# Kernel tuning notes

Hardware: AMD Instinct MI355X
Metric: run time of the kernel (lower is better)

The kernel has to match this reference:

```python
import jax, jax.numpy as jnp
import numpy as np

B, S, V, NC3, ND = 128, 200, 64, 4000, 100


def setup_inputs() -> dict:
    key = jax.random.key(0)
    ks = jax.random.split(key, 20)
    s = 0.05
    n = lambda k, shp: jax.random.normal(k, shp, dtype=jnp.float32) * s
    return {
        "c3_seq": jax.random.randint(ks[0], (B, S), 0, NC3),
        "d_seq": jax.random.randint(ks[1], (B, S), 0, ND),
        "r_seq": jax.random.randint(ks[2], (B, S), 0, 2),
        "v_c3": n(ks[3], (V,)),
        "D_w": n(ks[4], (ND, 1)),
        "v_d": n(ks[5], (V,)),
        "R_w": n(ks[6], (2, V)),
        "W_ih": n(ks[7], (3 * V, 2 * V)),
        "W_hh": n(ks[8], (3 * V, V)),
        "b_ih": n(ks[9], (3 * V,)),
        "b_hh": n(ks[10], (3 * V,)),
        "l1_w1": n(ks[11], (V, V)),
        "l1_b1": n(ks[12], (V,)),
        "l1_w2": n(ks[13], (1, V)),
        "l1_b2": n(ks[14], (1,)),
        "l2_w1": n(ks[15], (V, 3 * V)),
        "l2_b1": n(ks[16], (V,)),
        "l2_w2": n(ks[17], (1, V)),
        "l2_b2": n(ks[18], (1,)),
    }


def _forward(c3_seq, d_seq, r_seq, v_c3, D_w, v_d, R_w, W_ih, W_hh, b_ih, b_hh,
             l1_w1, l1_b1, l1_w2, l1_b2, l2_w1, l2_b1, l2_w2, l2_b2):
    B_, S_ = c3_seq.shape
    V_ = v_c3.shape[0]
    gamma_seq = D_w[d_seq]                       # [B,S,1]
    v_d_seq = gamma_seq * v_d                    # [B,S,V]
    v_r_seq = R_w[r_seq]                         # [B,S,V]
    x = jnp.concatenate([v_d_seq, v_r_seq], axis=-1)  # [B,S,2V]
    xg = x @ W_ih.T + b_ih                       # precompute GRU input gates [B,S,3V]

    # time-major for scan
    tm = lambda a: jnp.swapaxes(a, 0, 1)
    xg_t, gamma_t = tm(xg), tm(gamma_seq[..., 0])
    r_t, c3_t = tm(r_seq), tm(c3_seq)
    vd_t, vr_t = tm(v_d_seq), tm(v_r_seq)
    rows = jnp.arange(B_)

    def mlp1(h):  # linear_1 (dropout = identity in eval)
        return (jax.nn.relu(h @ l1_w1.T + l1_b1) @ l1_w2.T + l1_b2)[:, 0]

    def mlp2(z):  # linear_2
        return (jax.nn.relu(z @ l2_w1.T + l2_b1) @ l2_w2.T + l2_b2)[:, 0]

    h0 = jnp.zeros((B_, V_), xg.dtype)
    alpha0 = jnp.zeros((B_,), xg.dtype)
    C3_init = jnp.zeros((B_, NC3), xg.dtype)

    def step(carry, inputs):
        h, alpha, C3 = carry
        xg_i, gamma, r, c3, vdi, vri = inputs
        # GRU cell (torch gate order: r, z, n)
        hg = h @ W_hh.T + b_hh
        rg = jax.nn.sigmoid(xg_i[:, :V_] + hg[:, :V_])
        zg = jax.nn.sigmoid(xg_i[:, V_:2 * V_] + hg[:, V_:2 * V_])
        ng = jnp.tanh(xg_i[:, 2 * V_:] + rg * hg[:, 2 * V_:])
        h = (1.0 - zg) * ng + zg * h
        # alpha update
        alpha_new = mlp1(h)
        cond = (alpha - gamma) >= 0
        alpha = jnp.where(r == 1,
                          jnp.where(cond, alpha_new, alpha),
                          jnp.where(cond, alpha, alpha_new))
        # gather -> tiny MLP -> scatter
        beta = C3[rows, c3]                              # [B]
        z = jnp.concatenate([beta[:, None] * v_c3, vdi, vri], axis=-1)  # [B,3V]
        new_c3 = mlp2(z)
        C3 = C3.at[rows, c3].set(new_c3)
        return (h, alpha, C3), (h, alpha, C3)

    _, (h_seq, alpha_seq, C3_seq) = jax.lax.scan(
        step, (h0, alpha0, C3_init), (xg_t, gamma_t, r_t, c3_t, vd_t, vr_t))
    return tm(alpha_seq), tm(h_seq), tm(C3_seq)


def reference(c3_seq, d_seq, r_seq, v_c3, D_w, v_d, R_w, W_ih, W_hh, b_ih, b_hh,
              l1_w1, l1_b1, l1_w2, l1_b2, l2_w1, l2_b1, l2_w2, l2_b2):
    return _forward(c3_seq, d_seq, r_seq, v_c3, D_w, v_d, R_w, W_ih, W_hh, b_ih, b_hh,
                    l1_w1, l1_b1, l1_w2, l1_b2, l2_w1, l2_b1, l2_w2, l2_b2)
```

## Files before the change

### kernel.cpp

```cpp
#include <hip/hip_runtime.h>
#include <math.h>

#define Bn 128
#define Sn 200
#define NC3n 4000
#define GRUB Bn
#define FILLB (Bn * 4)

typedef float vf4 __attribute__((ext_vector_type(4)));

__device__ __forceinline__ float fexp(float x) { return __builtin_amdgcn_exp2f(x * 1.44269504f); }
__device__ __forceinline__ float frcp(float x) { return __builtin_amdgcn_rcpf(x); }
__device__ __forceinline__ float fsig(float x) { return frcp(1.f + fexp(-x)); }
__device__ __forceinline__ float rlanef(float v, int k) {
    return __int_as_float(__builtin_amdgcn_readlane(__float_as_int(v), k));
}
__device__ __forceinline__ void nt_store4(float* p, float4 q) {
    vf4 v; v.x = q.x; v.y = q.y; v.z = q.z; v.w = q.w;
    __builtin_nontemporal_store(v, (vf4*)p);
}
__device__ __forceinline__ void lds_barrier() {
    __builtin_amdgcn_sched_barrier(0);
    asm volatile("s_waitcnt lgkmcnt(0)" ::: "memory");
    __builtin_amdgcn_s_barrier();
    __builtin_amdgcn_sched_barrier(0);
}

#define UPD(q, cbase) { int d = cc - (cbase); if ((unsigned)d < 4u) { \
    q.x = (d==0)?v:q.x; q.y = (d==1)?v:q.y; q.z = (d==2)?v:q.z; q.w = (d==3)?v:q.w; } }

struct GruLds {
    float pPart[Sn][68];
    float hbc[4][64];
    float u[192], w0[192], w1[192];
    float hg[2][192];
    float gam[Sn];
    int   r[Sn];
};
struct FillLds {
    float gam[Sn], val[Sn];
    int   r[Sn], c3[Sn], succ[Sn], root[Sn];
    float A[64], Bv[64], C0[64], C1[64], W2[64];
    float l2b2;
};

__global__ __launch_bounds__(256, 2) void fused11_kernel(
    const int* __restrict__ c3_seq, const int* __restrict__ d_seq,
    const int* __restrict__ r_seq, const float* __restrict__ v_c3,
    const float* __restrict__ D_w, const float* __restrict__ v_d,
    const float* __restrict__ R_w, const float* __restrict__ W_ih,
    const float* __restrict__ W_hh, const float* __restrict__ b_ih,
    const float* __restrict__ b_hh,
    const float* __restrict__ l1_w1, const float* __restrict__ l1_b1,
    const float* __restrict__ l1_w2, const float* __restrict__ l1_b2,
    const float* __restrict__ l2_w1, const float* __restrict__ l2_b1,
    const float* __restrict__ l2_w2, const float* __restrict__ l2_b2,
    float* __restrict__ out_alpha, float* __restrict__ out_h,
    float* __restrict__ out_c3)
{
    __shared__ __align__(16) union { GruLds g; FillLds f; } S;

    const int tid = threadIdx.x;
    const int bid = blockIdx.x;

    if (bid < GRUB) {
        __builtin_amdgcn_s_setprio(1);
        const int b    = bid;
        const int role = tid >> 6;
        const int j    = tid & 63;

        if (tid < Sn) {
            S.g.gam[tid] = D_w[d_seq[b * Sn + tid]];
            S.g.r[tid]   = r_seq[b * Sn + tid];
        }
        if (tid < 192) {
            const float4* rp  = (const float4*)(W_ih + (size_t)tid * 128);
            const float4* vd4 = (const float4*)v_d;
            const float4* q04 = (const float4*)R_w;
            const float4* q14 = (const float4*)(R_w + 64);
            float u = 0.f, w0 = 0.f, w1 = 0.f;
            #pragma unroll 4
            for (int k = 0; k < 16; ++k) {
                float4 a  = rp[k];
                float4 bb = rp[16 + k];
                float4 vd = vd4[k], q0 = q04[k], q1 = q14[k];
                u  += a.x*vd.x + a.y*vd.y + a.z*vd.z + a.w*vd.w;
                w0 += bb.x*q0.x + bb.y*q0.y + bb.z*q0.z + bb.w*q0.w;
                w1 += bb.x*q1.x + bb.y*q1.y + bb.z*q1.z + bb.w*q1.w;
            }
            float bih = b_ih[tid];
            S.g.u[tid]  = u;
            S.g.w0[tid] = w0 + bih;
            S.g.w1[tid] = w1 + bih;
        }
        float w[64];
        {
            const float* src = (role < 3) ? (W_hh + (size_t)(role * 64 + j) * 64)
                                          : (l1_w1 + (size_t)j * 64);
            const float4* s4 = (const float4*)src;
            #pragma unroll
            for (int k = 0; k < 16; ++k) {
                float4 v = s4[k];
                w[4*k+0]=v.x; w[4*k+1]=v.y; w[4*k+2]=v.z; w[4*k+3]=v.w;
            }
        }
        #pragma unroll
        for (int k = 0; k < 16; ++k)
            asm volatile("" : "+v"(w[4*k+0]), "+v"(w[4*k+1]), "+v"(w[4*k+2]), "+v"(w[4*k+3]));

        float bown = 0.f, l1b = 0.f, l1w2v = 0.f;
        if (role < 3) {
            bown = b_hh[role * 64 + j];
            S.g.hg[0][role * 64 + j] = bown;
        } else {
            l1b = l1_b1[j]; l1w2v = l1_w2[j];
        }
        const float l1b2c = l1_b2[0];
        __syncthreads();

        const float uj  = S.g.u[j],  u1  = S.g.u[64+j],  u2  = S.g.u[128+j];
        const float w00 = S.g.w0[j], w01 = S.g.w0[64+j], w02 = S.g.w0[128+j];
        const float w10 = S.g.w1[j], w11 = S.g.w1[64+j], w12 = S.g.w1[128+j];

        float vh = 0.f;
        float* outp = out_h + (size_t)b * Sn * 64 + j;
        float gamc = S.g.gam[0];
        int   rc   = S.g.r[0];

        for (int t = 0; t < Sn; ++t) {
            const int buf = t & 1;
            float hr = S.g.hg[buf][j], hz = S.g.hg[buf][64+j], hn = S.g.hg[buf][128+j];
            float gam = gamc;
            int   r   = rc;
            float rg = fsig(fmaf(gam, uj, r ? w10 : w00) + hr);
            float zg = fsig(fmaf(gam, u1, r ? w11 : w01) + hz);
            float e2 = fexp(2.f * (fmaf(gam, u2, r ? w12 : w02) + rg * hn));
            float ng = 1.f - 2.f * frcp(e2 + 1.f);
            vh = (1.f - zg) * ng + zg * vh;
            S.g.hbc[role][j] = vh;
            if (role == 3) { outp[0] = vh; outp += 64; }
            float4 hreg[16];
            #pragma unroll
            for (int k = 0; k < 16; ++k)
                hreg[k] = *(const float4*)&S.g.hbc[role][k * 4];
            __builtin_amdgcn_sched_barrier(0);
            if (t + 1 < Sn) { gamc = S.g.gam[t + 1]; rc = S.g.r[t + 1]; }
            float a0=0.f, a1=0.f, a2=0.f, a3=0.f;
            #pragma unroll
            for (int k = 0; k < 16; ++k) {
                a0 = fmaf(w[4*k+0], hreg[k].x, a0);
                a1 = fmaf(w[4*k+1], hreg[k].y, a1);
                a2 = fmaf(w[4*k+2], hreg[k].z, a2);
                a3 = fmaf(w[4*k+3], hreg[k].w, a3);
            }
            float dot = (a0 + a1) + (a2 + a3);
            if (role < 3) {
                S.g.hg[buf ^ 1][role * 64 + j] = bown + dot;
            } else {
                S.g.pPart[t][j] = fmaxf(dot + l1b, 0.f) * l1w2v;
            }
            lds_barrier();
        }
        if (role == 3) {
            const int j3 = (j < 8) ? (192 + j) : 199;
            float4 s0 = make_float4(0.f,0.f,0.f,0.f), s1 = s0, s2 = s0, s3 = s0;
            const float4* p0 = (const float4*)&S.g.pPart[j][0];
            const float4* p1 = (const float4*)&S.g.pPart[64 + j][0];
            const float4* p2 = (const float4*)&S.g.pPart[128 + j][0];
            const float4* p3 = (const float4*)&S.g.pPart[j3][0];
            #pragma unroll
            for (int k = 0; k < 16; ++k) {
                float4 a = p0[k], bq = p1[k], c = p2[k], d = p3[k];
                s0.x += a.x;  s0.y += a.y;  s0.z += a.z;  s0.w += a.w;
                s1.x += bq.x; s1.y += bq.y; s1.z += bq.z; s1.w += bq.w;
                s2.x += c.x;  s2.y += c.y;  s2.z += c.z;  s2.w += c.w;
                s3.x += d.x;  s3.y += d.y;  s3.z += d.z;  s3.w += d.w;
            }
            float an0 = ((s0.x+s0.y)+(s0.z+s0.w)) + l1b2c;
            float an1 = ((s1.x+s1.y)+(s1.z+s1.w)) + l1b2c;
            float an2 = ((s2.x+s2.y)+(s2.z+s2.w)) + l1b2c;
            float an3 = ((s3.x+s3.y)+(s3.z+s3.w)) + l1b2c;
            float g0 = S.g.gam[j],       g1 = S.g.gam[64 + j];
            float g2 = S.g.gam[128 + j], g3 = S.g.gam[j3];
            int   r0 = S.g.r[j],         r1 = S.g.r[64 + j];
            int   r2 = S.g.r[128 + j],   r3 = S.g.r[j3];
            float alpha = 0.f;
            float* oa = out_alpha + b * Sn;
            for (int t = 0; t < Sn; ++t) {
                const int q = t >> 6, l = t & 63;
                float an, g; int rr;
                if (q == 0)      { an = rlanef(an0,l); g = rlanef(g0,l); rr = __builtin_amdgcn_readlane(r0,l); }
                else if (q == 1) { an = rlanef(an1,l); g = rlanef(g1,l); rr = __builtin_amdgcn_readlane(r1,l); }
                else if (q == 2) { an = rlanef(an2,l); g = rlanef(g2,l); rr = __builtin_amdgcn_readlane(r2,l); }
                else             { an = rlanef(an3,l); g = rlanef(g3,l); rr = __builtin_amdgcn_readlane(r3,l); }
                bool cond = (alpha - g) >= 0.f;
                alpha = rr ? (cond ? an : alpha) : (cond ? alpha : an);
                if (j == 0) oa[t] = alpha;
            }
        }
    } else {
        const int fb = bid - GRUB;
        const int b  = fb >> 2;
        const int qt = fb & 3;
        if (tid < Sn) {
            S.f.gam[tid] = D_w[d_seq[b*Sn + tid]];
            S.f.r[tid]   = r_seq[b*Sn + tid];
            S.f.c3[tid]  = c3_seq[b*Sn + tid];
        }
        if (tid < 64) {
            const float4* row4 = (const float4*)(l2_w1 + (size_t)tid * 192);
            const float4* vc4  = (const float4*)v_c3;
            const float4* vd4  = (const float4*)v_d;
            const float4* q04  = (const float4*)R_w;
            const float4* q14  = (const float4*)(R_w + 64);
            float a2=0.f, b2=0.f, c0=0.f, c1=0.f;
            #pragma unroll 4
            for (int k = 0; k < 16; ++k) {
                float4 ra = row4[k], rb = row4[16+k], rc = row4[32+k];
                float4 vc = vc4[k], vd = vd4[k], q0 = q04[k], q1 = q14[k];
                a2 += ra.x*vc.x + ra.y*vc.y + ra.z*vc.z + ra.w*vc.w;
                b2 += rb.x*vd.x + rb.y*vd.y + rb.z*vd.z + rb.w*vd.w;
                c0 += rc.x*q0.x + rc.y*q0.y + rc.z*q0.z + rc.w*q0.w;
                c1 += rc.x*q1.x + rc.y*q1.y + rc.z*q1.z + rc.w*q1.w;
            }
            S.f.A[tid]  = a2;
            S.f.Bv[tid] = b2;
            S.f.C0[tid] = c0 + l2_b1[tid];
            S.f.C1[tid] = c1 + l2_b1[tid];
            S.f.W2[tid] = l2_w2[tid];
        }
        if (tid == 0) S.f.l2b2 = l2_b2[0];
        __syncthreads();
        if (tid < Sn) {
            int c = S.f.c3[tid];
            int s = -1;
            for (int u = tid + 1; u < Sn; ++u)
                if (S.f.c3[u] == c) { s = u; break; }
            S.f.succ[tid] = s;
            int rt = 1;
            for (int u = 0; u < tid; ++u)
                if (S.f.c3[u] == c) { rt = 0; break; }
            S.f.root[tid] = rt;
        }
        __syncthreads();
        {
            const int g  = tid >> 4;
            const int l  = tid & 15;
            const int j0 = l * 4;
            float A0=S.f.A[j0],  A1=S.f.A[j0+1],  A2=S.f.A[j0+2],  A3=S.f.A[j0+3];
            float B0=S.f.Bv[j0], B1=S.f.Bv[j0+1], B2=S.f.Bv[j0+2], B3=S.f.Bv[j0+3];
            float C00=S.f.C0[j0],C01=S.f.C0[j0+1],C02=S.f.C0[j0+2],C03=S.f.C0[j0+3];
            float C10=S.f.C1[j0],C11=S.f.C1[j0+1],C12=S.f.C1[j0+2],C13=S.f.C1[j0+3];
            float W0=S.f.W2[j0], W1=S.f.W2[j0+1], W2v=S.f.W2[j0+2],W3=S.f.W2[j0+3];
            float l2b2 = S.f.l2b2;
            for (int t0 = g; t0 < Sn; t0 += 16) {
                if (!S.f.root[t0]) continue;
                float beta = 0.f;
                int t = t0;
                while (t >= 0) {
                    float gam = S.f.gam[t];
                    int   r   = S.f.r[t];
                    float s = W0*fmaxf(A0*beta + B0*gam + (r ? C10 : C00), 0.f)
                            + W1*fmaxf(A1*beta + B1*gam + (r ? C11 : C01), 0.f)
                            + W2v*fmaxf(A2*beta + B2*gam + (r ? C12 : C02), 0.f)
                            + W3*fmaxf(A3*beta + B3*gam + (r ? C13 : C03), 0.f);
                    s += __shfl_xor(s, 1, 16);
                    s += __shfl_xor(s, 2, 16);
                    s += __shfl_xor(s, 4, 16);
                    s += __shfl_xor(s, 8, 16);
                    beta = s + l2b2;
                    if (l == 0) S.f.val[t] = beta;
                    t = S.f.succ[t];
                }
            }
        }
        __syncthreads();
        const int cA = tid*4, cB = 1024 + tid*4, cC = 2048 + tid*4, cD = 3072 + tid*4;
        float4 qA = make_float4(0.f,0.f,0.f,0.f), qB = qA, qC = qA, qD = qA;
        const int t0 = qt * 50;
        for (int t = 0; t < t0; ++t) {
            int cc = S.f.c3[t]; float v = S.f.val[t];
            UPD(qA, cA) UPD(qB, cB) UPD(qC, cC) UPD(qD, cD)
        }
        float* rowp = out_c3 + (size_t)b * Sn * NC3n + (size_t)t0 * NC3n;
        const bool doD = (tid < 232);
        for (int t = t0; t < t0 + 50; ++t) {
            int cc = S.f.c3[t]; float v = S.f.val[t];
            UPD(qA, cA) UPD(qB, cB) UPD(qC, cC) UPD(qD, cD)
            nt_store4(rowp + cA, qA);
            nt_store4(rowp + cB, qB);
            nt_store4(rowp + cC, qC);
            if (doD) nt_store4(rowp + cD, qD);
            rowp += NC3n;
        }
    }
}

extern "C" void kernel_launch(void* const* d_in, const int* in_sizes, int n_in,
                              void* d_out, int out_size, void* d_ws, size_t ws_size,
                              hipStream_t stream)
{
    const int*   c3_seq = (const int*)  d_in[0];
    const int*   d_seq  = (const int*)  d_in[1];
    const int*   r_seq  = (const int*)  d_in[2];
    const float* v_c3   = (const float*)d_in[3];
    const float* D_w    = (const float*)d_in[4];
    const float* v_d    = (const float*)d_in[5];
    const float* R_w    = (const float*)d_in[6];
    const float* W_ih   = (const float*)d_in[7];
    const float* W_hh   = (const float*)d_in[8];
    const float* b_ih   = (const float*)d_in[9];
    const float* b_hh   = (const float*)d_in[10];
    const float* l1_w1  = (const float*)d_in[11];
    const float* l1_b1  = (const float*)d_in[12];
    const float* l1_w2  = (const float*)d_in[13];
    const float* l1_b2  = (const float*)d_in[14];
    const float* l2_w1  = (const float*)d_in[15];
    const float* l2_b1  = (const float*)d_in[16];
    const float* l2_w2  = (const float*)d_in[17];
    const float* l2_b2  = (const float*)d_in[18];

    float* out_alpha = (float*)d_out;
    float* out_h     = out_alpha + Bn*Sn;
    float* out_c3    = out_h + (size_t)Bn*Sn*64;

    fused11_kernel<<<GRUB + FILLB, 256, 0, stream>>>(
        c3_seq, d_seq, r_seq, v_c3, D_w, v_d, R_w, W_ih, W_hh, b_ih, b_hh,
        l1_w1, l1_b1, l1_w2, l1_b2, l2_w1, l2_b1, l2_w2, l2_b2,
        out_alpha, out_h, out_c3);
}
```

Measured before the change: 151.4 us.

## Process two batch rows per GRU block and rebalance fill blocks into thirds

Each GRU block now runs two independent batch recurrences interleaved, so the per-step matvec and barrier are shared across two rows and only 64 GRU blocks are launched. The per-step MLP1 partial sums are stored in LDS as bf16 to fit both rows, and the C3 fill work is split into three time ranges per batch instead of four, giving fewer blocks. This aims to hide latency in the serial GRU chain and cut block count, but doubles per-step work on the critical path and adds bf16 rounding error in alpha.

```diff
diff --git a/kernel.cpp b/kernel.cpp
--- a/kernel.cpp
+++ b/kernel.cpp
@@ -4,8 +4,8 @@
 #define Bn 128
 #define Sn 200
 #define NC3n 4000
-#define GRUB Bn
-#define FILLB (Bn * 4)
+#define GRUB 64
+#define FILLB (Bn * 3)
 
 typedef float vf4 __attribute__((ext_vector_type(4)));
 
@@ -25,17 +25,21 @@
     __builtin_amdgcn_s_barrier();
     __builtin_amdgcn_sched_barrier(0);
 }
+__device__ __forceinline__ unsigned short f2bf(float f) {
+    unsigned u = __float_as_uint(f);
+    return (unsigned short)((u + 0x7FFFu + ((u >> 16) & 1u)) >> 16);
+}
 
 #define UPD(q, cbase) { int d = cc - (cbase); if ((unsigned)d < 4u) { \
     q.x = (d==0)?v:q.x; q.y = (d==1)?v:q.y; q.z = (d==2)?v:q.z; q.w = (d==3)?v:q.w; } }
 
 struct GruLds {
-    float pPart[Sn][68];
-    float hbc[4][64];
+    float hbc[2][4][64];
     float u[192], w0[192], w1[192];
-    float hg[2][192];
-    float gam[Sn];
-    int   r[Sn];
+    float hg[2][2][192];
+    float gam[2][Sn];
+    int   r[2][Sn];
+    unsigned short pPart[2][Sn][64];
 };
 struct FillLds {
     float gam[Sn], val[Sn];
@@ -44,7 +48,7 @@
     float l2b2;
 };
 
-__global__ __launch_bounds__(256, 2) void fused11_kernel(
+__global__ __launch_bounds__(256, 2) void fused12_kernel(
     const int* __restrict__ c3_seq, const int* __restrict__ d_seq,
     const int* __restrict__ r_seq, const float* __restrict__ v_c3,
     const float* __restrict__ D_w, const float* __restrict__ v_d,
@@ -65,13 +69,15 @@
 
     if (bid < GRUB) {
         __builtin_amdgcn_s_setprio(1);
-        const int b    = bid;
         const int role = tid >> 6;
         const int j    = tid & 63;
 
-        if (tid < Sn) {
-            S.g.gam[tid] = D_w[d_seq[b * Sn + tid]];
-            S.g.r[tid]   = r_seq[b * Sn + tid];
+        for (int i = tid; i < 2 * Sn; i += 256) {
+            int rw2 = (i >= Sn) ? 1 : 0;
+            int t2  = i - rw2 * Sn;
+            int bb  = bid * 2 + rw2;
+            S.g.gam[rw2][t2] = D_w[d_seq[bb * Sn + t2]];
+            S.g.r[rw2][t2]   = r_seq[bb * Sn + t2];
         }
         if (tid < 192) {
             const float4* rp  = (const float4*)(W_ih + (size_t)tid * 128);
@@ -111,7 +117,8 @@
         float bown = 0.f, l1b = 0.f, l1w2v = 0.f;
         if (role < 3) {
             bown = b_hh[role * 64 + j];
-            S.g.hg[0][role * 64 + j] = bown;
+            S.g.hg[0][0][role * 64 + j] = bown;
+            S.g.hg[1][0][role * 64 + j] = bown;
         } else {
             l1b = l1_b1[j]; l1w2v = l1_w2[j];
         }
@@ -122,86 +129,103 @@
         const float w00 = S.g.w0[j], w01 = S.g.w0[64+j], w02 = S.g.w0[128+j];
         const float w10 = S.g.w1[j], w11 = S.g.w1[64+j], w12 = S.g.w1[128+j];
 
-        float vh = 0.f;
-        float* outp = out_h + (size_t)b * Sn * 64 + j;
-        float gamc = S.g.gam[0];
-        int   rc   = S.g.r[0];
+        float vh0 = 0.f, vh1 = 0.f;
+        float* outp = out_h + (size_t)(bid * 2 + ((role == 1) ? 1 : 0)) * Sn * 64 + j;
+        float gamc0 = S.g.gam[0][0], gamc1 = S.g.gam[1][0];
+        int   rc0   = S.g.r[0][0],   rc1   = S.g.r[1][0];
 
         for (int t = 0; t < Sn; ++t) {
             const int buf = t & 1;
-            float hr = S.g.hg[buf][j], hz = S.g.hg[buf][64+j], hn = S.g.hg[buf][128+j];
-            float gam = gamc;
-            int   r   = rc;
-            float rg = fsig(fmaf(gam, uj, r ? w10 : w00) + hr);
-            float zg = fsig(fmaf(gam, u1, r ? w11 : w01) + hz);
-            float e2 = fexp(2.f * (fmaf(gam, u2, r ? w12 : w02) + rg * hn));
-            float ng = 1.f - 2.f * frcp(e2 + 1.f);
-            vh = (1.f - zg) * ng + zg * vh;
-            S.g.hbc[role][j] = vh;
-            if (role == 3) { outp[0] = vh; outp += 64; }
-            float4 hreg[16];
-            #pragma unroll
-            for (int k = 0; k < 16; ++k)
-                hreg[k] = *(const float4*)&S.g.hbc[role][k * 4];
+            float hr0 = S.g.hg[0][buf][j], hz0 = S.g.hg[0][buf][64+j], hn0 = S.g.hg[0][buf][128+j];
+            float hr1 = S.g.hg[1][buf][j], hz1 = S.g.hg[1][buf][64+j], hn1 = S.g.hg[1][buf][128+j];
+            float rg0 = fsig(fmaf(gamc0, uj, rc0 ? w10 : w00) + hr0);
+            float zg0 = fsig(fmaf(gamc0, u1, rc0 ? w11 : w01) + hz0);
+            float e20 = fexp(2.f * (fmaf(gamc0, u2, rc0 ? w12 : w02) + rg0 * hn0));
+            float ng0 = 1.f - 2.f * frcp(e20 + 1.f);
+            vh0 = (1.f - zg0) * ng0 + zg0 * vh0;
+            float rg1 = fsig(fmaf(gamc1, uj, rc1 ? w10 : w00) + hr1);
+            float zg1 = fsig(fmaf(gamc1, u1, rc1 ? w11 : w01) + hz1);
+            float e21 = fexp(2.f * (fmaf(gamc1, u2, rc1 ? w12 : w02) + rg1 * hn1));
+            float ng1 = 1.f - 2.f * frcp(e21 + 1.f);
+            vh1 = (1.f - zg1) * ng1 + zg1 * vh1;
+            S.g.hbc[0][role][j] = vh0;
+            S.g.hbc[1][role][j] = vh1;
+            if (role == 0) { outp[0] = vh0; outp += 64; }
+            if (role == 1) { outp[0] = vh1; outp += 64; }
+            float4 h0[16], h1[16];
+            #pragma unroll
+            for (int k = 0; k < 16; ++k) h0[k] = *(const float4*)&S.g.hbc[0][role][k * 4];
+            #pragma unroll
+            for (int k = 0; k < 16; ++k) h1[k] = *(const float4*)&S.g.hbc[1][role][k * 4];
             __builtin_amdgcn_sched_barrier(0);
-            if (t + 1 < Sn) { gamc = S.g.gam[t + 1]; rc = S.g.r[t + 1]; }
+            if (t + 1 < Sn) {
+                gamc0 = S.g.gam[0][t + 1]; rc0 = S.g.r[0][t + 1];
+                gamc1 = S.g.gam[1][t + 1]; rc1 = S.g.r[1][t + 1];
+            }
             float a0=0.f, a1=0.f, a2=0.f, a3=0.f;
+            float b0=0.f, b1=0.f, b2=0.f, b3=0.f;
             #pragma unroll
             for (int k = 0; k < 16; ++k) {
-                a0 = fmaf(w[4*k+0], hreg[k].x, a0);
-                a1 = fmaf(w[4*k+1], hreg[k].y, a1);
-                a2 = fmaf(w[4*k+2], hreg[k].z, a2);
-                a3 = fmaf(w[4*k+3], hreg[k].w, a3);
-            }
-            float dot = (a0 + a1) + (a2 + a3);
+                a0 = fmaf(w[4*k+0], h0[k].x, a0); a1 = fmaf(w[4*k+1], h0[k].y, a1);
+                a2 = fmaf(w[4*k+2], h0[k].z, a2); a3 = fmaf(w[4*k+3], h0[k].w, a3);
+                b0 = fmaf(w[4*k+0], h1[k].x, b0); b1 = fmaf(w[4*k+1], h1[k].y, b1);
+                b2 = fmaf(w[4*k+2], h1[k].z, b2); b3 = fmaf(w[4*k+3], h1[k].w, b3);
+            }
+            float dot0 = (a0 + a1) + (a2 + a3);
+            float dot1 = (b0 + b1) + (b2 + b3);
             if (role < 3) {
-                S.g.hg[buf ^ 1][role * 64 + j] = bown + dot;
+                S.g.hg[0][buf ^ 1][role * 64 + j] = bown + dot0;
+                S.g.hg[1][buf ^ 1][role * 64 + j] = bown + dot1;
             } else {
-                S.g.pPart[t][j] = fmaxf(dot + l1b, 0.f) * l1w2v;
+                S.g.pPart[0][t][j] = f2bf(fmaxf(dot0 + l1b, 0.f) * l1w2v);
+                S.g.pPart[1][t][j] = f2bf(fmaxf(dot1 + l1b, 0.f) * l1w2v);
             }
             lds_barrier();
         }
-        if (role == 3) {
+        if (role >= 2) {
+            const int rw = (role == 3) ? 0 : 1;
+            const int b  = bid * 2 + rw;
             const int j3 = (j < 8) ? (192 + j) : 199;
-            float4 s0 = make_float4(0.f,0.f,0.f,0.f), s1 = s0, s2 = s0, s3 = s0;
-            const float4* p0 = (const float4*)&S.g.pPart[j][0];
-            const float4* p1 = (const float4*)&S.g.pPart[64 + j][0];
-            const float4* p2 = (const float4*)&S.g.pPart[128 + j][0];
-            const float4* p3 = (const float4*)&S.g.pPart[j3][0];
-            #pragma unroll
-            for (int k = 0; k < 16; ++k) {
-                float4 a = p0[k], bq = p1[k], c = p2[k], d = p3[k];
-                s0.x += a.x;  s0.y += a.y;  s0.z += a.z;  s0.w += a.w;
-                s1.x += bq.x; s1.y += bq.y; s1.z += bq.z; s1.w += bq.w;
-                s2.x += c.x;  s2.y += c.y;  s2.z += c.z;  s2.w += c.w;
-                s3.x += d.x;  s3.y += d.y;  s3.z += d.z;  s3.w += d.w;
-            }
-            float an0 = ((s0.x+s0.y)+(s0.z+s0.w)) + l1b2c;
-            float an1 = ((s1.x+s1.y)+(s1.z+s1.w)) + l1b2c;
-            float an2 = ((s2.x+s2.y)+(s2.z+s2.w)) + l1b2c;
-            float an3 = ((s3.x+s3.y)+(s3.z+s3.w)) + l1b2c;
-            float g0 = S.g.gam[j],       g1 = S.g.gam[64 + j];
-            float g2 = S.g.gam[128 + j], g3 = S.g.gam[j3];
-            int   r0 = S.g.r[j],         r1 = S.g.r[64 + j];
-            int   r2 = S.g.r[128 + j],   r3 = S.g.r[j3];
+            const int ts0 = j, ts1 = 64 + j, ts2 = 128 + j, ts3 = j3;
+            float an[4];
+            int tss[4] = {ts0, ts1, ts2, ts3};
+            #pragma unroll
+            for (int q = 0; q < 4; ++q) {
+                const uint4* pp = (const uint4*)&S.g.pPart[rw][tss[q]][0];
+                float s = 0.f;
+                #pragma unroll
+                for (int k = 0; k < 8; ++k) {
+                    uint4 v = pp[k];
+                    s += __uint_as_float(v.x << 16) + __uint_as_float(v.x & 0xFFFF0000u);
+                    s += __uint_as_float(v.y << 16) + __uint_as_float(v.y & 0xFFFF0000u);
+                    s += __uint_as_float(v.z << 16) + __uint_as_float(v.z & 0xFFFF0000u);
+                    s += __uint_as_float(v.w << 16) + __uint_as_float(v.w & 0xFFFF0000u);
+                }
+                an[q] = s + l1b2c;
+            }
+            float an0 = an[0], an1 = an[1], an2 = an[2], an3 = an[3];
+            float g0 = S.g.gam[rw][ts0], g1 = S.g.gam[rw][ts1];
+            float g2 = S.g.gam[rw][ts2], g3 = S.g.gam[rw][ts3];
+            int   r0 = S.g.r[rw][ts0],   r1 = S.g.r[rw][ts1];
+            int   r2 = S.g.r[rw][ts2],   r3 = S.g.r[rw][ts3];
             float alpha = 0.f;
             float* oa = out_alpha + b * Sn;
             for (int t = 0; t < Sn; ++t) {
                 const int q = t >> 6, l = t & 63;
-                float an, g; int rr;
-                if (q == 0)      { an = rlanef(an0,l); g = rlanef(g0,l); rr = __builtin_amdgcn_readlane(r0,l); }
-                else if (q == 1) { an = rlanef(an1,l); g = rlanef(g1,l); rr = __builtin_amdgcn_readlane(r1,l); }
-                else if (q == 2) { an = rlanef(an2,l); g = rlanef(g2,l); rr = __builtin_amdgcn_readlane(r2,l); }
-                else             { an = rlanef(an3,l); g = rlanef(g3,l); rr = __builtin_amdgcn_readlane(r3,l); }
+                float anv, g; int rr;
+                if (q == 0)      { anv = rlanef(an0,l); g = rlanef(g0,l); rr = __builtin_amdgcn_readlane(r0,l); }
+                else if (q == 1) { anv = rlanef(an1,l); g = rlanef(g1,l); rr = __builtin_amdgcn_readlane(r1,l); }
+                else if (q == 2) { anv = rlanef(an2,l); g = rlanef(g2,l); rr = __builtin_amdgcn_readlane(r2,l); }
+                else             { anv = rlanef(an3,l); g = rlanef(g3,l); rr = __builtin_amdgcn_readlane(r3,l); }
                 bool cond = (alpha - g) >= 0.f;
-                alpha = rr ? (cond ? an : alpha) : (cond ? alpha : an);
+                alpha = rr ? (cond ? anv : alpha) : (cond ? alpha : anv);
                 if (j == 0) oa[t] = alpha;
             }
         }
     } else {
         const int fb = bid - GRUB;
-        const int b  = fb >> 2;
-        const int qt = fb & 3;
+        const int b  = fb / 3;
+        const int th = fb - b * 3;
         if (tid < Sn) {
             S.f.gam[tid] = D_w[d_seq[b*Sn + tid]];
             S.f.r[tid]   = r_seq[b*Sn + tid];
@@ -275,16 +299,17 @@
             }
         }
         __syncthreads();
+        const int t0 = (th == 0) ? 0 : (th == 1 ? 67 : 134);
+        const int t1 = (th == 0) ? 67 : (th == 1 ? 134 : 200);
         const int cA = tid*4, cB = 1024 + tid*4, cC = 2048 + tid*4, cD = 3072 + tid*4;
         float4 qA = make_float4(0.f,0.f,0.f,0.f), qB = qA, qC = qA, qD = qA;
-        const int t0 = qt * 50;
         for (int t = 0; t < t0; ++t) {
             int cc = S.f.c3[t]; float v = S.f.val[t];
             UPD(qA, cA) UPD(qB, cB) UPD(qC, cC) UPD(qD, cD)
         }
         float* rowp = out_c3 + (size_t)b * Sn * NC3n + (size_t)t0 * NC3n;
         const bool doD = (tid < 232);
-        for (int t = t0; t < t0 + 50; ++t) {
+        for (int t = t0; t < t1; ++t) {
             int cc = S.f.c3[t]; float v = S.f.val[t];
             UPD(qA, cA) UPD(qB, cB) UPD(qC, cC) UPD(qD, cD)
             nt_store4(rowp + cA, qA);
@@ -324,7 +349,7 @@
     float* out_h     = out_alpha + Bn*Sn;
     float* out_c3    = out_h + (size_t)Bn*Sn*64;
 
-    fused11_kernel<<<GRUB + FILLB, 256, 0, stream>>>(
+    fused12_kernel<<<GRUB + FILLB, 256, 0, stream>>>(
         c3_seq, d_seq, r_seq, v_c3, D_w, v_d, R_w, W_ih, W_hh, b_ih, b_hh,
         l1_w1, l1_b1, l1_w2, l1_b2, l2_w1, l2_b1, l2_w2, l2_b2,
         out_alpha, out_h, out_c3);
```

Result: slower. 197.4 us (+30.4%).

## Run GRU recurrence in a single wavefront to drop per-step block barriers

Applied to the files above, without the earlier changes.

The GRU recurrence moves from four cooperating wavefronts joined by a block barrier each step to a single 64-lane wavefront. Each lane keeps the r and z gate weight rows in registers and reads the n-gate and MLP weight rows from padded LDS, computing all four dot products itself. The alpha-MLP partials are stored in LDS as bf16, and occupancy is dropped to one block per CU. This removes the barrier and LDS handoff latency on the serial critical path, but quadruples the per-lane work per step and adds bf16 rounding to the alpha inputs.

```diff
diff --git a/kernel.cpp b/kernel.cpp
--- a/kernel.cpp
+++ b/kernel.cpp
@@ -19,23 +19,22 @@
     vf4 v; v.x = q.x; v.y = q.y; v.z = q.z; v.w = q.w;
     __builtin_nontemporal_store(v, (vf4*)p);
 }
-__device__ __forceinline__ void lds_barrier() {
-    __builtin_amdgcn_sched_barrier(0);
-    asm volatile("s_waitcnt lgkmcnt(0)" ::: "memory");
-    __builtin_amdgcn_s_barrier();
-    __builtin_amdgcn_sched_barrier(0);
+__device__ __forceinline__ unsigned short f2bf(float f) {
+    unsigned u = __float_as_uint(f);
+    return (unsigned short)((u + 0x7FFFu + ((u >> 16) & 1u)) >> 16);
 }
 
 #define UPD(q, cbase) { int d = cc - (cbase); if ((unsigned)d < 4u) { \
     q.x = (d==0)?v:q.x; q.y = (d==1)?v:q.y; q.z = (d==2)?v:q.z; q.w = (d==3)?v:q.w; } }
 
 struct GruLds {
-    float pPart[Sn][68];
-    float hbc[4][64];
+    float wnp[64 * 65];
+    float l1p[64 * 65];
+    unsigned short pPart[Sn * 64];
     float u[192], w0[192], w1[192];
-    float hg[2][192];
     float gam[Sn];
     int   r[Sn];
+    float hbc[64];
 };
 struct FillLds {
     float gam[Sn], val[Sn];
@@ -44,7 +43,7 @@
     float l2b2;
 };
 
-__global__ __launch_bounds__(256, 2) void fused11_kernel(
+__global__ __launch_bounds__(256, 1) void fused13_kernel(
     const int* __restrict__ c3_seq, const int* __restrict__ d_seq,
     const int* __restrict__ r_seq, const float* __restrict__ v_c3,
     const float* __restrict__ D_w, const float* __restrict__ v_d,
@@ -64,10 +63,9 @@
     const int bid = blockIdx.x;
 
     if (bid < GRUB) {
-        __builtin_amdgcn_s_setprio(1);
-        const int b    = bid;
-        const int role = tid >> 6;
-        const int j    = tid & 63;
+        const int b   = bid;
+        const int wid = tid >> 6;
+        const int j   = tid & 63;
 
         if (tid < Sn) {
             S.g.gam[tid] = D_w[d_seq[b * Sn + tid]];
@@ -93,93 +91,114 @@
             S.g.w0[tid] = w0 + bih;
             S.g.w1[tid] = w1 + bih;
         }
-        float w[64];
+        if (wid == 1) {
+            const int jj = tid - 64;
+            const float4* s4 = (const float4*)(W_hh + (size_t)(128 + jj) * 64);
+            #pragma unroll
+            for (int k = 0; k < 16; ++k) {
+                float4 v = s4[k];
+                S.g.wnp[jj * 65 + 4*k+0] = v.x;
+                S.g.wnp[jj * 65 + 4*k+1] = v.y;
+                S.g.wnp[jj * 65 + 4*k+2] = v.z;
+                S.g.wnp[jj * 65 + 4*k+3] = v.w;
+            }
+        }
+        if (wid == 2) {
+            const int jj = tid - 128;
+            const float4* s4 = (const float4*)(l1_w1 + (size_t)jj * 64);
+            #pragma unroll
+            for (int k = 0; k < 16; ++k) {
+                float4 v = s4[k];
+                S.g.l1p[jj * 65 + 4*k+0] = v.x;
+                S.g.l1p[jj * 65 + 4*k+1] = v.y;
+                S.g.l1p[jj * 65 + 4*k+2] = v.z;
+                S.g.l1p[jj * 65 + 4*k+3] = v.w;
+            }
+        }
+        __syncthreads();
+        if (tid >= 64) return;
+
+        float wr[64], wz[64];
         {
-            const float* src = (role < 3) ? (W_hh + (size_t)(role * 64 + j) * 64)
-                                          : (l1_w1 + (size_t)j * 64);
-            const float4* s4 = (const float4*)src;
-            #pragma unroll
-            for (int k = 0; k < 16; ++k) {
-                float4 v = s4[k];
-                w[4*k+0]=v.x; w[4*k+1]=v.y; w[4*k+2]=v.z; w[4*k+3]=v.w;
+            const float4* r0 = (const float4*)(W_hh + (size_t)j * 64);
+            const float4* r1 = (const float4*)(W_hh + (size_t)(64 + j) * 64);
+            #pragma unroll
+            for (int k = 0; k < 16; ++k) {
+                float4 a = r0[k], c = r1[k];
+                wr[4*k+0]=a.x; wr[4*k+1]=a.y; wr[4*k+2]=a.z; wr[4*k+3]=a.w;
+                wz[4*k+0]=c.x; wz[4*k+1]=c.y; wz[4*k+2]=c.z; wz[4*k+3]=c.w;
             }
         }
         #pragma unroll
-        for (int k = 0; k < 16; ++k)
-            asm volatile("" : "+v"(w[4*k+0]), "+v"(w[4*k+1]), "+v"(w[4*k+2]), "+v"(w[4*k+3]));
-
-        float bown = 0.f, l1b = 0.f, l1w2v = 0.f;
-        if (role < 3) {
-            bown = b_hh[role * 64 + j];
-            S.g.hg[0][role * 64 + j] = bown;
-        } else {
-            l1b = l1_b1[j]; l1w2v = l1_w2[j];
-        }
-        const float l1b2c = l1_b2[0];
-        __syncthreads();
-
+        for (int k = 0; k < 16; ++k) {
+            asm volatile("" : "+v"(wr[4*k+0]), "+v"(wr[4*k+1]), "+v"(wr[4*k+2]), "+v"(wr[4*k+3]));
+            asm volatile("" : "+v"(wz[4*k+0]), "+v"(wz[4*k+1]), "+v"(wz[4*k+2]), "+v"(wz[4*k+3]));
+        }
+        const float bhr = b_hh[j], bhz = b_hh[64 + j], bhn = b_hh[128 + j];
+        const float l1b = l1_b1[j], l1w2v = l1_w2[j], l1b2c = l1_b2[0];
         const float uj  = S.g.u[j],  u1  = S.g.u[64+j],  u2  = S.g.u[128+j];
         const float w00 = S.g.w0[j], w01 = S.g.w0[64+j], w02 = S.g.w0[128+j];
         const float w10 = S.g.w1[j], w11 = S.g.w1[64+j], w12 = S.g.w1[128+j];
 
+        float hgr = bhr, hgz = bhz, hgn = bhn;
         float vh = 0.f;
         float* outp = out_h + (size_t)b * Sn * 64 + j;
+        const float* wnrow = &S.g.wnp[j * 65];
+        const float* l1row = &S.g.l1p[j * 65];
         float gamc = S.g.gam[0];
         int   rc   = S.g.r[0];
 
         for (int t = 0; t < Sn; ++t) {
-            const int buf = t & 1;
-            float hr = S.g.hg[buf][j], hz = S.g.hg[buf][64+j], hn = S.g.hg[buf][128+j];
-            float gam = gamc;
-            int   r   = rc;
-            float rg = fsig(fmaf(gam, uj, r ? w10 : w00) + hr);
-            float zg = fsig(fmaf(gam, u1, r ? w11 : w01) + hz);
-            float e2 = fexp(2.f * (fmaf(gam, u2, r ? w12 : w02) + rg * hn));
+            float gam = gamc; int r = rc;
+            float rg = fsig(fmaf(gam, uj, r ? w10 : w00) + hgr);
+            float zg = fsig(fmaf(gam, u1, r ? w11 : w01) + hgz);
+            float e2 = fexp(2.f * (fmaf(gam, u2, r ? w12 : w02) + rg * hgn));
             float ng = 1.f - 2.f * frcp(e2 + 1.f);
             vh = (1.f - zg) * ng + zg * vh;
-            S.g.hbc[role][j] = vh;
-            if (role == 3) { outp[0] = vh; outp += 64; }
-            float4 hreg[16];
-            #pragma unroll
-            for (int k = 0; k < 16; ++k)
-                hreg[k] = *(const float4*)&S.g.hbc[role][k * 4];
-            __builtin_amdgcn_sched_barrier(0);
+            S.g.hbc[j] = vh;
+            outp[0] = vh; outp += 64;
             if (t + 1 < Sn) { gamc = S.g.gam[t + 1]; rc = S.g.r[t + 1]; }
-            float a0=0.f, a1=0.f, a2=0.f, a3=0.f;
-            #pragma unroll
-            for (int k = 0; k < 16; ++k) {
-                a0 = fmaf(w[4*k+0], hreg[k].x, a0);
-                a1 = fmaf(w[4*k+1], hreg[k].y, a1);
-                a2 = fmaf(w[4*k+2], hreg[k].z, a2);
-                a3 = fmaf(w[4*k+3], hreg[k].w, a3);
-            }
-            float dot = (a0 + a1) + (a2 + a3);
-            if (role < 3) {
-                S.g.hg[buf ^ 1][role * 64 + j] = bown + dot;
-            } else {
-                S.g.pPart[t][j] = fmaxf(dot + l1b, 0.f) * l1w2v;
-            }
-            lds_barrier();
-        }
-        if (role == 3) {
+            float r0=0.f,r1=0.f, z0=0.f,z1=0.f, n0=0.f,n1=0.f, p0=0.f,p1=0.f;
+            #pragma unroll
+            for (int k4 = 0; k4 < 16; ++k4) {
+                float4 hq = *(const float4*)&S.g.hbc[k4 * 4];
+                float wn0 = wnrow[4*k4+0], wn1 = wnrow[4*k4+1];
+                float wn2 = wnrow[4*k4+2], wn3 = wnrow[4*k4+3];
+                float lq0 = l1row[4*k4+0], lq1 = l1row[4*k4+1];
+                float lq2 = l1row[4*k4+2], lq3 = l1row[4*k4+3];
+                r0 = fmaf(wr[4*k4+0], hq.x, r0); r1 = fmaf(wr[4*k4+1], hq.y, r1);
+                r0 = fmaf(wr[4*k4+2], hq.z, r0); r1 = fmaf(wr[4*k4+3], hq.w, r1);
+                z0 = fmaf(wz[4*k4+0], hq.x, z0); z1 = fmaf(wz[4*k4+1], hq.y, z1);
+                z0 = fmaf(wz[4*k4+2], hq.z, z0); z1 = fmaf(wz[4*k4+3], hq.w, z1);
+                n0 = fmaf(wn0, hq.x, n0); n1 = fmaf(wn1, hq.y, n1);
+                n0 = fmaf(wn2, hq.z, n0); n1 = fmaf(wn3, hq.w, n1);
+                p0 = fmaf(lq0, hq.x, p0); p1 = fmaf(lq1, hq.y, p1);
+                p0 = fmaf(lq2, hq.z, p0); p1 = fmaf(lq3, hq.w, p1);
+            }
+            hgr = bhr + (r0 + r1);
+            hgz = bhz + (z0 + z1);
+            hgn = bhn + (n0 + n1);
+            S.g.pPart[t * 64 + j] = f2bf(fmaxf((p0 + p1) + l1b, 0.f) * l1w2v);
+        }
+        {
             const int j3 = (j < 8) ? (192 + j) : 199;
-            float4 s0 = make_float4(0.f,0.f,0.f,0.f), s1 = s0, s2 = s0, s3 = s0;
-            const float4* p0 = (const float4*)&S.g.pPart[j][0];
-            const float4* p1 = (const float4*)&S.g.pPart[64 + j][0];
-            const float4* p2 = (const float4*)&S.g.pPart[128 + j][0];
-            const float4* p3 = (const float4*)&S.g.pPart[j3][0];
-            #pragma unroll
-            for (int k = 0; k < 16; ++k) {
-                float4 a = p0[k], bq = p1[k], c = p2[k], d = p3[k];
-                s0.x += a.x;  s0.y += a.y;  s0.z += a.z;  s0.w += a.w;
-                s1.x += bq.x; s1.y += bq.y; s1.z += bq.z; s1.w += bq.w;
-                s2.x += c.x;  s2.y += c.y;  s2.z += c.z;  s2.w += c.w;
-                s3.x += d.x;  s3.y += d.y;  s3.z += d.z;  s3.w += d.w;
-            }
-            float an0 = ((s0.x+s0.y)+(s0.z+s0.w)) + l1b2c;
-            float an1 = ((s1.x+s1.y)+(s1.z+s1.w)) + l1b2c;
-            float an2 = ((s2.x+s2.y)+(s2.z+s2.w)) + l1b2c;
-            float an3 = ((s3.x+s3.y)+(s3.z+s3.w)) + l1b2c;
+            const int tss[4] = { j, 64 + j, 128 + j, j3 };
+            float an[4];
+            #pragma unroll
+            for (int q = 0; q < 4; ++q) {
+                const uint4* pp = (const uint4*)&S.g.pPart[tss[q] * 64];
+                float s = 0.f;
+                #pragma unroll
+                for (int k = 0; k < 8; ++k) {
+                    uint4 v = pp[k];
+                    s += __uint_as_float(v.x << 16) + __uint_as_float(v.x & 0xFFFF0000u);
+                    s += __uint_as_float(v.y << 16) + __uint_as_float(v.y & 0xFFFF0000u);
+                    s += __uint_as_float(v.z << 16) + __uint_as_float(v.z & 0xFFFF0000u);
+                    s += __uint_as_float(v.w << 16) + __uint_as_float(v.w & 0xFFFF0000u);
+                }
+                an[q] = s + l1b2c;
+            }
+            float an0 = an[0], an1 = an[1], an2 = an[2], an3 = an[3];
             float g0 = S.g.gam[j],       g1 = S.g.gam[64 + j];
             float g2 = S.g.gam[128 + j], g3 = S.g.gam[j3];
             int   r0 = S.g.r[j],         r1 = S.g.r[64 + j];
@@ -188,13 +207,13 @@
             float* oa = out_alpha + b * Sn;
             for (int t = 0; t < Sn; ++t) {
                 const int q = t >> 6, l = t & 63;
-                float an, g; int rr;
-                if (q == 0)      { an = rlanef(an0,l); g = rlanef(g0,l); rr = __builtin_amdgcn_readlane(r0,l); }
-                else if (q == 1) { an = rlanef(an1,l); g = rlanef(g1,l); rr = __builtin_amdgcn_readlane(r1,l); }
-                else if (q == 2) { an = rlanef(an2,l); g = rlanef(g2,l); rr = __builtin_amdgcn_readlane(r2,l); }
-                else             { an = rlanef(an3,l); g = rlanef(g3,l); rr = __builtin_amdgcn_readlane(r3,l); }
+                float anv, g; int rr;
+                if (q == 0)      { anv = rlanef(an0,l); g = rlanef(g0,l); rr = __builtin_amdgcn_readlane(r0,l); }
+                else if (q == 1) { anv = rlanef(an1,l); g = rlanef(g1,l); rr = __builtin_amdgcn_readlane(r1,l); }
+                else if (q == 2) { anv = rlanef(an2,l); g = rlanef(g2,l); rr = __builtin_amdgcn_readlane(r2,l); }
+                else             { anv = rlanef(an3,l); g = rlanef(g3,l); rr = __builtin_amdgcn_readlane(r3,l); }
                 bool cond = (alpha - g) >= 0.f;
-                alpha = rr ? (cond ? an : alpha) : (cond ? alpha : an);
+                alpha = rr ? (cond ? anv : alpha) : (cond ? alpha : anv);
                 if (j == 0) oa[t] = alpha;
             }
         }
@@ -324,7 +343,7 @@
     float* out_h     = out_alpha + Bn*Sn;
     float* out_c3    = out_h + (size_t)Bn*Sn*64;
 
-    fused11_kernel<<<GRUB + FILLB, 256, 0, stream>>>(
+    fused13_kernel<<<GRUB + FILLB, 256, 0, stream>>>(
         c3_seq, d_seq, r_seq, v_c3, D_w, v_d, R_w, W_ih, W_hh, b_ih, b_hh,
         l1_w1, l1_b1, l1_w2, l1_b2, l2_w1, l2_b1, l2_w2, l2_b2,
         out_alpha, out_h, out_c3);
```

Result: slower. 250.6 us (+65.5%).
